# Optimization experiments

Hardware: AMD Instinct MI355X
Metric: run time of the kernel (lower is better)

## Reference

```python
import jax, jax.numpy as jnp
import numpy as np


def setup_inputs() -> dict:
    key = jax.random.key(0)
    ks = jax.random.split(key, 5)
    d_model = 1024
    B, S = 4, 2048
    scale = 1.0 / np.sqrt(d_model)
    return {
        "num_heads": 16,
        "q_proj_weight": jax.random.normal(ks[0], (d_model, d_model), jnp.float32) * scale,
        "k_proj_weight": jax.random.normal(ks[1], (d_model, d_model), jnp.float32) * scale,
        "v_proj_weight": jax.random.normal(ks[2], (d_model, d_model), jnp.float32) * scale,
        "o_proj_weight": jax.random.normal(ks[3], (d_model, d_model), jnp.float32) * scale,
        "in_features": jax.random.normal(ks[4], (B, S, d_model), jnp.float32),
    }


def reference(num_heads, q_proj_weight, k_proj_weight, v_proj_weight, o_proj_weight, in_features):
    B, S, d_in = in_features.shape
    d_k = q_proj_weight.shape[-2] // num_heads
    d_v = v_proj_weight.shape[-2] // num_heads
    # QKV projections: x @ W.T, then split heads -> [B, H, S, d]
    q = (in_features @ q_proj_weight.T).reshape(B, S, num_heads, d_k).transpose(0, 2, 1, 3)
    k = (in_features @ k_proj_weight.T).reshape(B, S, num_heads, d_k).transpose(0, 2, 1, 3)
    v = (in_features @ v_proj_weight.T).reshape(B, S, num_heads, d_v).transpose(0, 2, 1, 3)
    # causal scaled dot-product attention
    scores = jnp.einsum("bhqd,bhkd->bhqk", q, k) / jnp.sqrt(jnp.asarray(d_k, q.dtype))
    causal = jnp.tril(jnp.ones((S, S), dtype=bool))
    scores = jnp.where(causal, scores, jnp.asarray(-jnp.inf, scores.dtype))
    probs = jax.nn.softmax(scores, axis=-1)
    attn = jnp.einsum("bhqk,bhkd->bhqd", probs, v)  # [B, H, S, d_v]
    concat = attn.transpose(0, 2, 1, 3).reshape(B, S, num_heads * d_v)
    return concat @ o_proj_weight.T
```

## Files before the change

kernel.cpp:

```cpp
#include <hip/hip_runtime.h>
#include <hip/hip_bf16.h>
#include <cstdint>
#include <cstddef>

typedef short bf16x8 __attribute__((ext_vector_type(8)));
typedef float f32x4 __attribute__((ext_vector_type(4)));
typedef float f32x16 __attribute__((ext_vector_type(16)));
typedef unsigned short u16x4 __attribute__((ext_vector_type(4)));

__device__ __forceinline__ unsigned short f2bf(float f) {
  unsigned int u = __builtin_bit_cast(unsigned int, f);
  u = (u + 0x7FFFu + ((u >> 16) & 1u)) >> 16;
  return (unsigned short)u;
}

__device__ __forceinline__ f32x4 mfma16x16x32(bf16x8 a, bf16x8 b, f32x4 c) {
  return __builtin_amdgcn_mfma_f32_16x16x32_bf16(a, b, c, 0, 0, 0);
}
__device__ __forceinline__ f32x16 mfma32x32x16(bf16x8 a, bf16x8 b, f32x16 c) {
  return __builtin_amdgcn_mfma_f32_32x32x16_bf16(a, b, c, 0, 0, 0);
}

constexpr int KSTRIDE = 1056;
constexpr int VSTRIDE = 2080;

__global__ __launch_bounds__(256) void cvt_f32_bf16(const float* __restrict__ src,
                                                    unsigned short* __restrict__ dst, int n) {
  int i = (blockIdx.x * 256 + threadIdx.x) * 4;
  if (i + 3 < n) {
    float4 v = *reinterpret_cast<const float4*>(src + i);
    u16x4 o;
    o[0] = f2bf(v.x); o[1] = f2bf(v.y); o[2] = f2bf(v.z); o[3] = f2bf(v.w);
    *reinterpret_cast<u16x4*>(dst + i) = o;
  }
}

template <int OUTMODE>
__global__ __launch_bounds__(256) void gemm_bt(const unsigned short* __restrict__ A,
                                               const unsigned short* __restrict__ Bw,
                                               void* __restrict__ Cp,
                                               int M, int N, int K) {
  __shared__ unsigned short As[128 * 32];
  __shared__ unsigned short Bs[128 * 32];
  const int tid  = threadIdx.x;
  const int lane = tid & 63, wid = tid >> 6;
  const int g = lane >> 4, cc = lane & 15;
  const int wr = wid >> 1, wc = wid & 1;
  const int m0 = blockIdx.y * 128, n0 = blockIdx.x * 128;
  const int arow = tid >> 2;
  const int acol = (tid & 3) * 8;

  const unsigned short* gA = A  + (size_t)(m0 + arow) * K + acol;
  const unsigned short* gB = Bw + (size_t)(n0 + arow) * K + acol;

  f32x4 acc[4][4];
#pragma unroll
  for (int i = 0; i < 4; ++i)
#pragma unroll
    for (int j = 0; j < 4; ++j) acc[i][j] = f32x4{0.f, 0.f, 0.f, 0.f};

  for (int k0 = 0; k0 < K; k0 += 32) {
    __builtin_amdgcn_global_load_lds(
        (const __attribute__((address_space(1))) void*)(gA + k0),
        (__attribute__((address_space(3))) void*)(As + wid * 512), 16, 0, 0);
    __builtin_amdgcn_global_load_lds(
        (const __attribute__((address_space(1))) void*)(gA + (size_t)64 * K + k0),
        (__attribute__((address_space(3))) void*)(As + 2048 + wid * 512), 16, 0, 0);
    __builtin_amdgcn_global_load_lds(
        (const __attribute__((address_space(1))) void*)(gB + k0),
        (__attribute__((address_space(3))) void*)(Bs + wid * 512), 16, 0, 0);
    __builtin_amdgcn_global_load_lds(
        (const __attribute__((address_space(1))) void*)(gB + (size_t)64 * K + k0),
        (__attribute__((address_space(3))) void*)(Bs + 2048 + wid * 512), 16, 0, 0);
    __syncthreads();

    bf16x8 af[4], bfv[4];
#pragma unroll
    for (int mi = 0; mi < 4; ++mi)
      af[mi] = *reinterpret_cast<const bf16x8*>(As + (wr * 64 + mi * 16 + cc) * 32 + g * 8);
#pragma unroll
    for (int ni = 0; ni < 4; ++ni)
      bfv[ni] = *reinterpret_cast<const bf16x8*>(Bs + (wc * 64 + ni * 16 + cc) * 32 + g * 8);
#pragma unroll
    for (int mi = 0; mi < 4; ++mi)
#pragma unroll
      for (int ni = 0; ni < 4; ++ni)
        acc[mi][ni] = mfma16x16x32(af[mi], bfv[ni], acc[mi][ni]);
    __syncthreads();
  }

#pragma unroll
  for (int mi = 0; mi < 4; ++mi) {
#pragma unroll
    for (int ni = 0; ni < 4; ++ni) {
      const int row0 = m0 + wr * 64 + mi * 16 + g * 4;
      const int col  = n0 + wc * 64 + ni * 16 + cc;
      if (OUTMODE == 2) {
        u16x4 o;
#pragma unroll
        for (int r = 0; r < 4; ++r) o[r] = f2bf(acc[mi][ni][r]);
        const size_t idx = ((size_t)(row0 >> 11) * 1024 + col) * VSTRIDE + (row0 & 2047);
        *reinterpret_cast<u16x4*>(reinterpret_cast<unsigned short*>(Cp) + idx) = o;
      } else {
#pragma unroll
        for (int r = 0; r < 4; ++r) {
          const int row = row0 + r;
          if (OUTMODE == 1)
            reinterpret_cast<float*>(Cp)[(size_t)row * N + col] = acc[mi][ni][r];
          else if (OUTMODE == 3)
            reinterpret_cast<unsigned short*>(Cp)[(size_t)row * N + col] = f2bf(acc[mi][ni][r] * 0.125f);
          else if (OUTMODE == 4)
            reinterpret_cast<unsigned short*>(Cp)[(size_t)row * KSTRIDE + col] = f2bf(acc[mi][ni][r]);
          else
            reinterpret_cast<unsigned short*>(Cp)[(size_t)row * N + col] = f2bf(acc[mi][ni][r]);
        }
      }
    }
  }
}

__global__ __launch_bounds__(256) void attn_fwd(const unsigned short* __restrict__ Q,
                                                const unsigned short* __restrict__ Kp,
                                                const unsigned short* __restrict__ Vt,
                                                unsigned short* __restrict__ O) {
  constexpr int S = 2048, DM = 1024;
  __shared__ unsigned short Kl[2][64 * 64];
  __shared__ unsigned short Vl[2][64 * 64];
  const int tid  = threadIdx.x;
  const int lane = tid & 63, wid = tid >> 6;
  const int l31 = lane & 31, hi = lane >> 5;
  const int pr = blockIdx.x & 7;
  const int h  = (blockIdx.x >> 3) & 15;
  const int b  = blockIdx.x >> 7;

  const size_t baseQ = (size_t)b * S * DM + (size_t)h * 64;
  const unsigned short* Kbh = Kp + (size_t)b * S * KSTRIDE + (size_t)h * 64;
  const unsigned short* Vbh = Vt + (size_t)((b * 16 + h) * 64) * VSTRIDE;

  const int r0 = wid * 8 + (lane >> 3);
  const int sc = lane & 7;
  const int c0 = (sc ^ (r0 & 7)) * 8;
  const int c1 = (sc ^ ((r0 + 32) & 7)) * 8;
  const int swz = (l31 & 7);

  auto STAGE = [&](int bf, int t) {
    const int kv0 = t * 64;
    __builtin_amdgcn_global_load_lds(
        (const __attribute__((address_space(1))) void*)(Kbh + (size_t)(kv0 + r0) * KSTRIDE + c0),
        (__attribute__((address_space(3))) void*)(&Kl[bf][wid * 512]), 16, 0, 0);
    __builtin_amdgcn_global_load_lds(
        (const __attribute__((address_space(1))) void*)(Kbh + (size_t)(kv0 + r0 + 32) * KSTRIDE + c1),
        (__attribute__((address_space(3))) void*)(&Kl[bf][2048 + wid * 512]), 16, 0, 0);
    __builtin_amdgcn_global_load_lds(
        (const __attribute__((address_space(1))) void*)(Vbh + (size_t)r0 * VSTRIDE + kv0 + c0),
        (__attribute__((address_space(3))) void*)(&Vl[bf][wid * 512]), 16, 0, 0);
    __builtin_amdgcn_global_load_lds(
        (const __attribute__((address_space(1))) void*)(Vbh + (size_t)(r0 + 32) * VSTRIDE + kv0 + c1),
        (__attribute__((address_space(3))) void*)(&Vl[bf][2048 + wid * 512]), 16, 0, 0);
  };

  int cur = 0;
  for (int half = 0; half < 2; ++half) {
    const int bqt = half ? (15 - pr) : pr;
    const int qw  = bqt * 128 + wid * 32;

    const unsigned short* Qrow = Q + baseQ + (size_t)(qw + l31) * DM + hi * 8;
    bf16x8 qf[4];
#pragma unroll
    for (int m = 0; m < 4; ++m) qf[m] = *reinterpret_cast<const bf16x8*>(Qrow + m * 16);

    f32x16 acc0, acc1;
#pragma unroll
    for (int i = 0; i < 16; ++i) { acc0[i] = 0.f; acc1[i] = 0.f; }
    float m_st = -3.0e38f, l_st = 0.f;

    const int nt = bqt * 2 + 2;
    STAGE(cur, 0);
    __syncthreads();

    for (int t = 0; t < nt; ++t) {
      if (t + 1 < nt) STAGE(cur ^ 1, t + 1);
      const int kv0 = t * 64;

#pragma unroll
      for (int ss = 0; ss < 2; ++ss) {
        const int kvs = kv0 + ss * 32;
        if (kvs <= qw) {
          f32x16 s;
#pragma unroll
          for (int i = 0; i < 16; ++i) s[i] = 0.f;
#pragma unroll
          for (int m = 0; m < 4; ++m) {
            const bf16x8 a = *reinterpret_cast<const bf16x8*>(
                &Kl[cur][(ss * 32 + l31) * 64 + ((m * 2 + hi) ^ swz) * 8]);
            s = mfma32x32x16(a, qf[m], s);
          }

          float p[16];
          if (kvs == qw) {
#pragma unroll
            for (int r = 0; r < 16; ++r) {
              const int kvl = (r & 3) + 8 * (r >> 2) + 4 * hi;
              p[r] = (kvl <= l31) ? s[r] : -3.0e38f;
            }
          } else {
#pragma unroll
            for (int r = 0; r < 16; ++r) p[r] = s[r];
          }

          float tm = p[0];
#pragma unroll
          for (int r = 1; r < 16; ++r) tm = fmaxf(tm, p[r]);
          tm = fmaxf(tm, __shfl_xor(tm, 32));

          if (!__all(tm <= m_st)) {
            const float m_new = fmaxf(m_st, tm);
            const float corr  = __expf(m_st - m_new);
#pragma unroll
            for (int i = 0; i < 16; ++i) {
              const int qr = (i & 3) + 8 * (i >> 2) + 4 * hi;
              const float cr = __shfl(corr, qr);
              acc0[i] *= cr; acc1[i] *= cr;
            }
            l_st *= corr;
            m_st = m_new;
          }

          float ls = 0.f;
#pragma unroll
          for (int r = 0; r < 16; ++r) { p[r] = __expf(p[r] - m_st); ls += p[r]; }
          ls += __shfl_xor(ls, 32);
          l_st += ls;

#pragma unroll
          for (int ks = 0; ks < 2; ++ks) {
            const int bb = ks * 8;
            float u[4];
#pragma unroll
            for (int i = 0; i < 4; ++i) {
              const float tv = hi ? p[bb + i] : p[bb + 4 + i];
              u[i] = __shfl_xor(tv, 32);
            }
            bf16x8 pa;
#pragma unroll
            for (int j = 0; j < 4; ++j) {
              pa[j]     = (short)f2bf(hi ? u[j] : p[bb + j]);
              pa[4 + j] = (short)f2bf(hi ? p[bb + 4 + j] : u[j]);
            }
            const int ch = ss * 4 + ks * 2 + hi;
            const bf16x8 bv0 = *reinterpret_cast<const bf16x8*>(
                &Vl[cur][l31 * 64 + (ch ^ swz) * 8]);
            const bf16x8 bv1 = *reinterpret_cast<const bf16x8*>(
                &Vl[cur][(32 + l31) * 64 + (ch ^ swz) * 8]);
            acc0 = mfma32x32x16(pa, bv0, acc0);
            acc1 = mfma32x32x16(pa, bv1, acc1);
          }
        }
      }
      __syncthreads();
      cur ^= 1;
    }

    const float invl = 1.0f / l_st;
#pragma unroll
    for (int r = 0; r < 16; ++r) {
      const int qr = (r & 3) + 8 * (r >> 2) + 4 * hi;
      const float il = __shfl(invl, qr);
      unsigned short* Orow = O + baseQ + (size_t)(qw + qr) * DM;
      Orow[l31]      = f2bf(acc0[r] * il);
      Orow[32 + l31] = f2bf(acc1[r] * il);
    }
  }
}

extern "C" void kernel_launch(void* const* d_in, const int* in_sizes, int n_in,
                              void* d_out, int out_size, void* d_ws, size_t ws_size,
                              hipStream_t stream) {
  (void)in_sizes; (void)n_in; (void)out_size; (void)ws_size;
  constexpr int Bx = 4, S = 2048, DM = 1024;
  constexpr int M = Bx * S;
  constexpr size_t XEL = (size_t)M * DM;
  constexpr size_t WEL = (size_t)DM * DM;

  const float* Wq = (const float*)d_in[1];
  const float* Wk = (const float*)d_in[2];
  const float* Wv = (const float*)d_in[3];
  const float* Wo = (const float*)d_in[4];
  const float* Xf = (const float*)d_in[5];
  float* out = (float*)d_out;

  char* ws = (char*)d_ws;
  unsigned short* Xbf = (unsigned short*)(ws + 0);
  unsigned short* Qb  = (unsigned short*)(ws + 16777216);
  unsigned short* Kb  = (unsigned short*)(ws + 33554432);
  unsigned short* Vtb = (unsigned short*)(ws + 50855936);
  unsigned short* Wqb = (unsigned short*)(ws + 67895296);
  unsigned short* Wkb = (unsigned short*)(ws + 69992448);
  unsigned short* Wvb = (unsigned short*)(ws + 72089600);
  unsigned short* Wob = (unsigned short*)(ws + 74186752);
  unsigned short* Ob  = Xbf;

  cvt_f32_bf16<<<(int)(XEL / 1024), 256, 0, stream>>>(Xf, Xbf, (int)XEL);
  cvt_f32_bf16<<<(int)(WEL / 1024), 256, 0, stream>>>(Wq, Wqb, (int)WEL);
  cvt_f32_bf16<<<(int)(WEL / 1024), 256, 0, stream>>>(Wk, Wkb, (int)WEL);
  cvt_f32_bf16<<<(int)(WEL / 1024), 256, 0, stream>>>(Wv, Wvb, (int)WEL);
  cvt_f32_bf16<<<(int)(WEL / 1024), 256, 0, stream>>>(Wo, Wob, (int)WEL);

  dim3 gg(DM / 128, M / 128);
  gemm_bt<3><<<gg, 256, 0, stream>>>(Xbf, Wqb, Qb, M, DM, DM);
  gemm_bt<4><<<gg, 256, 0, stream>>>(Xbf, Wkb, Kb, M, DM, DM);
  gemm_bt<2><<<gg, 256, 0, stream>>>(Xbf, Wvb, Vtb, M, DM, DM);

  attn_fwd<<<Bx * 16 * 8, 256, 0, stream>>>(Qb, Kb, Vtb, Ob);

  gemm_bt<1><<<gg, 256, 0, stream>>>(Ob, Wob, out, M, DM, DM);
}
```

Baseline: 339.1 us.

## Fuse QKV GEMMs into one launch and double-buffer LDS tiles

Concatenates the Q, K and V weights into one buffer and runs a single GEMM with N=3072, routing each output tile to the Q, K or transposed-V layout by its column block. Both GEMM kernels now double-buffer LDS so the next k-tile's global-to-LDS loads are issued before the current tile's MFMAs. The four weight conversions are merged into one launch. This removes launch overhead and exposes load latency, at the cost of doubled LDS use per block, which may reduce occupancy.

```diff
diff --git a/kernel.cpp b/kernel.cpp
--- a/kernel.cpp
+++ b/kernel.cpp
@@ -35,13 +35,29 @@
   }
 }
 
-template <int OUTMODE>
-__global__ __launch_bounds__(256) void gemm_bt(const unsigned short* __restrict__ A,
-                                               const unsigned short* __restrict__ Bw,
-                                               void* __restrict__ Cp,
-                                               int M, int N, int K) {
-  __shared__ unsigned short As[128 * 32];
-  __shared__ unsigned short Bs[128 * 32];
+__global__ __launch_bounds__(256) void cvt_w4(const float* __restrict__ w0,
+                                              const float* __restrict__ w1,
+                                              const float* __restrict__ w2,
+                                              const float* __restrict__ w3,
+                                              unsigned short* __restrict__ dst) {
+  constexpr int WEL = 1024 * 1024;
+  int i = (blockIdx.x * 256 + threadIdx.x) * 4;
+  const int sel = i >> 20;
+  const float* src = sel == 0 ? w0 : sel == 1 ? w1 : sel == 2 ? w2 : w3;
+  float4 v = *reinterpret_cast<const float4*>(src + (i & (WEL - 1)));
+  u16x4 o;
+  o[0] = f2bf(v.x); o[1] = f2bf(v.y); o[2] = f2bf(v.z); o[3] = f2bf(v.w);
+  *reinterpret_cast<u16x4*>(dst + i) = o;
+}
+
+__global__ __launch_bounds__(256) void gemm_qkv(const unsigned short* __restrict__ A,
+                                                const unsigned short* __restrict__ Wf,
+                                                unsigned short* __restrict__ Qb,
+                                                unsigned short* __restrict__ Kb,
+                                                unsigned short* __restrict__ Vtb) {
+  constexpr int K = 1024;
+  __shared__ unsigned short As[2][128 * 32];
+  __shared__ unsigned short Bs[2][128 * 32];
   const int tid  = threadIdx.x;
   const int lane = tid & 63, wid = tid >> 6;
   const int g = lane >> 4, cc = lane & 15;
@@ -51,7 +67,7 @@
   const int acol = (tid & 3) * 8;
 
   const unsigned short* gA = A  + (size_t)(m0 + arow) * K + acol;
-  const unsigned short* gB = Bw + (size_t)(n0 + arow) * K + acol;
+  const unsigned short* gB = Wf + (size_t)(n0 + arow) * K + acol;
 
   f32x4 acc[4][4];
 #pragma unroll
@@ -59,34 +75,126 @@
 #pragma unroll
     for (int j = 0; j < 4; ++j) acc[i][j] = f32x4{0.f, 0.f, 0.f, 0.f};
 
-  for (int k0 = 0; k0 < K; k0 += 32) {
+  auto STAGE = [&](int bf, int k0) {
     __builtin_amdgcn_global_load_lds(
         (const __attribute__((address_space(1))) void*)(gA + k0),
-        (__attribute__((address_space(3))) void*)(As + wid * 512), 16, 0, 0);
+        (__attribute__((address_space(3))) void*)(&As[bf][wid * 512]), 16, 0, 0);
     __builtin_amdgcn_global_load_lds(
         (const __attribute__((address_space(1))) void*)(gA + (size_t)64 * K + k0),
-        (__attribute__((address_space(3))) void*)(As + 2048 + wid * 512), 16, 0, 0);
+        (__attribute__((address_space(3))) void*)(&As[bf][2048 + wid * 512]), 16, 0, 0);
     __builtin_amdgcn_global_load_lds(
         (const __attribute__((address_space(1))) void*)(gB + k0),
-        (__attribute__((address_space(3))) void*)(Bs + wid * 512), 16, 0, 0);
+        (__attribute__((address_space(3))) void*)(&Bs[bf][wid * 512]), 16, 0, 0);
     __builtin_amdgcn_global_load_lds(
         (const __attribute__((address_space(1))) void*)(gB + (size_t)64 * K + k0),
-        (__attribute__((address_space(3))) void*)(Bs + 2048 + wid * 512), 16, 0, 0);
-    __syncthreads();
-
+        (__attribute__((address_space(3))) void*)(&Bs[bf][2048 + wid * 512]), 16, 0, 0);
+  };
+
+  int cur = 0;
+  STAGE(0, 0);
+  __syncthreads();
+  for (int t = 0; t < K / 32; ++t) {
+    if (t + 1 < K / 32) STAGE(cur ^ 1, (t + 1) * 32);
     bf16x8 af[4], bfv[4];
 #pragma unroll
     for (int mi = 0; mi < 4; ++mi)
-      af[mi] = *reinterpret_cast<const bf16x8*>(As + (wr * 64 + mi * 16 + cc) * 32 + g * 8);
+      af[mi] = *reinterpret_cast<const bf16x8*>(&As[cur][(wr * 64 + mi * 16 + cc) * 32 + g * 8]);
 #pragma unroll
     for (int ni = 0; ni < 4; ++ni)
-      bfv[ni] = *reinterpret_cast<const bf16x8*>(Bs + (wc * 64 + ni * 16 + cc) * 32 + g * 8);
+      bfv[ni] = *reinterpret_cast<const bf16x8*>(&Bs[cur][(wc * 64 + ni * 16 + cc) * 32 + g * 8]);
 #pragma unroll
     for (int mi = 0; mi < 4; ++mi)
 #pragma unroll
       for (int ni = 0; ni < 4; ++ni)
         acc[mi][ni] = mfma16x16x32(af[mi], bfv[ni], acc[mi][ni]);
     __syncthreads();
+    cur ^= 1;
+  }
+
+  const int mode = n0 >> 10;
+  const int nh   = n0 & 1023;
+#pragma unroll
+  for (int mi = 0; mi < 4; ++mi) {
+#pragma unroll
+    for (int ni = 0; ni < 4; ++ni) {
+      const int row0 = m0 + wr * 64 + mi * 16 + g * 4;
+      const int col  = nh + wc * 64 + ni * 16 + cc;
+      if (mode == 2) {
+        u16x4 o;
+#pragma unroll
+        for (int r = 0; r < 4; ++r) o[r] = f2bf(acc[mi][ni][r]);
+        const size_t idx = ((size_t)(row0 >> 11) * 1024 + col) * VSTRIDE + (row0 & 2047);
+        *reinterpret_cast<u16x4*>(Vtb + idx) = o;
+      } else if (mode == 1) {
+#pragma unroll
+        for (int r = 0; r < 4; ++r)
+          Kb[(size_t)(row0 + r) * KSTRIDE + col] = f2bf(acc[mi][ni][r]);
+      } else {
+#pragma unroll
+        for (int r = 0; r < 4; ++r)
+          Qb[(size_t)(row0 + r) * 1024 + col] = f2bf(acc[mi][ni][r] * 0.125f);
+      }
+    }
+  }
+}
+
+__global__ __launch_bounds__(256) void gemm_op(const unsigned short* __restrict__ A,
+                                               const unsigned short* __restrict__ Bw,
+                                               float* __restrict__ Cp) {
+  constexpr int K = 1024, N = 1024;
+  __shared__ unsigned short As[2][128 * 32];
+  __shared__ unsigned short Bs[2][128 * 32];
+  const int tid  = threadIdx.x;
+  const int lane = tid & 63, wid = tid >> 6;
+  const int g = lane >> 4, cc = lane & 15;
+  const int wr = wid >> 1, wc = wid & 1;
+  const int m0 = blockIdx.y * 128, n0 = blockIdx.x * 128;
+  const int arow = tid >> 2;
+  const int acol = (tid & 3) * 8;
+
+  const unsigned short* gA = A  + (size_t)(m0 + arow) * K + acol;
+  const unsigned short* gB = Bw + (size_t)(n0 + arow) * K + acol;
+
+  f32x4 acc[4][4];
+#pragma unroll
+  for (int i = 0; i < 4; ++i)
+#pragma unroll
+    for (int j = 0; j < 4; ++j) acc[i][j] = f32x4{0.f, 0.f, 0.f, 0.f};
+
+  auto STAGE = [&](int bf, int k0) {
+    __builtin_amdgcn_global_load_lds(
+        (const __attribute__((address_space(1))) void*)(gA + k0),
+        (__attribute__((address_space(3))) void*)(&As[bf][wid * 512]), 16, 0, 0);
+    __builtin_amdgcn_global_load_lds(
+        (const __attribute__((address_space(1))) void*)(gA + (size_t)64 * K + k0),
+        (__attribute__((address_space(3))) void*)(&As[bf][2048 + wid * 512]), 16, 0, 0);
+    __builtin_amdgcn_global_load_lds(
+        (const __attribute__((address_space(1))) void*)(gB + k0),
+        (__attribute__((address_space(3))) void*)(&Bs[bf][wid * 512]), 16, 0, 0);
+    __builtin_amdgcn_global_load_lds(
+        (const __attribute__((address_space(1))) void*)(gB + (size_t)64 * K + k0),
+        (__attribute__((address_space(3))) void*)(&Bs[bf][2048 + wid * 512]), 16, 0, 0);
+  };
+
+  int cur = 0;
+  STAGE(0, 0);
+  __syncthreads();
+  for (int t = 0; t < K / 32; ++t) {
+    if (t + 1 < K / 32) STAGE(cur ^ 1, (t + 1) * 32);
+    bf16x8 af[4], bfv[4];
+#pragma unroll
+    for (int mi = 0; mi < 4; ++mi)
+      af[mi] = *reinterpret_cast<const bf16x8*>(&As[cur][(wr * 64 + mi * 16 + cc) * 32 + g * 8]);
+#pragma unroll
+    for (int ni = 0; ni < 4; ++ni)
+      bfv[ni] = *reinterpret_cast<const bf16x8*>(&Bs[cur][(wc * 64 + ni * 16 + cc) * 32 + g * 8]);
+#pragma unroll
+    for (int mi = 0; mi < 4; ++mi)
+#pragma unroll
+      for (int ni = 0; ni < 4; ++ni)
+        acc[mi][ni] = mfma16x16x32(af[mi], bfv[ni], acc[mi][ni]);
+    __syncthreads();
+    cur ^= 1;
   }
 
 #pragma unroll
@@ -95,26 +203,9 @@
     for (int ni = 0; ni < 4; ++ni) {
       const int row0 = m0 + wr * 64 + mi * 16 + g * 4;
       const int col  = n0 + wc * 64 + ni * 16 + cc;
-      if (OUTMODE == 2) {
-        u16x4 o;
-#pragma unroll
-        for (int r = 0; r < 4; ++r) o[r] = f2bf(acc[mi][ni][r]);
-        const size_t idx = ((size_t)(row0 >> 11) * 1024 + col) * VSTRIDE + (row0 & 2047);
-        *reinterpret_cast<u16x4*>(reinterpret_cast<unsigned short*>(Cp) + idx) = o;
-      } else {
-#pragma unroll
-        for (int r = 0; r < 4; ++r) {
-          const int row = row0 + r;
-          if (OUTMODE == 1)
-            reinterpret_cast<float*>(Cp)[(size_t)row * N + col] = acc[mi][ni][r];
-          else if (OUTMODE == 3)
-            reinterpret_cast<unsigned short*>(Cp)[(size_t)row * N + col] = f2bf(acc[mi][ni][r] * 0.125f);
-          else if (OUTMODE == 4)
-            reinterpret_cast<unsigned short*>(Cp)[(size_t)row * KSTRIDE + col] = f2bf(acc[mi][ni][r]);
-          else
-            reinterpret_cast<unsigned short*>(Cp)[(size_t)row * N + col] = f2bf(acc[mi][ni][r]);
-        }
-      }
+#pragma unroll
+      for (int r = 0; r < 4; ++r)
+        Cp[(size_t)(row0 + r) * N + col] = acc[mi][ni][r];
     }
   }
 }
@@ -280,7 +371,6 @@
   constexpr int Bx = 4, S = 2048, DM = 1024;
   constexpr int M = Bx * S;
   constexpr size_t XEL = (size_t)M * DM;
-  constexpr size_t WEL = (size_t)DM * DM;
 
   const float* Wq = (const float*)d_in[1];
   const float* Wk = (const float*)d_in[2];
@@ -294,24 +384,18 @@
   unsigned short* Qb  = (unsigned short*)(ws + 16777216);
   unsigned short* Kb  = (unsigned short*)(ws + 33554432);
   unsigned short* Vtb = (unsigned short*)(ws + 50855936);
-  unsigned short* Wqb = (unsigned short*)(ws + 67895296);
-  unsigned short* Wkb = (unsigned short*)(ws + 69992448);
-  unsigned short* Wvb = (unsigned short*)(ws + 72089600);
+  unsigned short* Wfb = (unsigned short*)(ws + 67895296);
   unsigned short* Wob = (unsigned short*)(ws + 74186752);
   unsigned short* Ob  = Xbf;
 
   cvt_f32_bf16<<<(int)(XEL / 1024), 256, 0, stream>>>(Xf, Xbf, (int)XEL);
-  cvt_f32_bf16<<<(int)(WEL / 1024), 256, 0, stream>>>(Wq, Wqb, (int)WEL);
-  cvt_f32_bf16<<<(int)(WEL / 1024), 256, 0, stream>>>(Wk, Wkb, (int)WEL);
-  cvt_f32_bf16<<<(int)(WEL / 1024), 256, 0, stream>>>(Wv, Wvb, (int)WEL);
-  cvt_f32_bf16<<<(int)(WEL / 1024), 256, 0, stream>>>(Wo, Wob, (int)WEL);
+  cvt_w4<<<4096, 256, 0, stream>>>(Wq, Wk, Wv, Wo, Wfb);
+
+  dim3 gq(3072 / 128, M / 128);
+  gemm_qkv<<<gq, 256, 0, stream>>>(Xbf, Wfb, Qb, Kb, Vtb);
+
+  attn_fwd<<<Bx * 16 * 8, 256, 0, stream>>>(Qb, Kb, Vtb, Ob);
 
   dim3 gg(DM / 128, M / 128);
-  gemm_bt<3><<<gg, 256, 0, stream>>>(Xbf, Wqb, Qb, M, DM, DM);
-  gemm_bt<4><<<gg, 256, 0, stream>>>(Xbf, Wkb, Kb, M, DM, DM);
-  gemm_bt<2><<<gg, 256, 0, stream>>>(Xbf, Wvb, Vtb, M, DM, DM);
-
-  attn_fwd<<<Bx * 16 * 8, 256, 0, stream>>>(Qb, Kb, Vtb, Ob);
-
-  gemm_bt<1><<<gg, 256, 0, stream>>>(Ob, Wob, out, M, DM, DM);
-}
+  gemm_op<<<gg, 256, 0, stream>>>(Ob, Wob, out);
+}
```

Result: faster. 312.5 us (-7.8%).
